# Performance work log

Measured on AMD Instinct MI355X. Metric: run time of the kernel, lower is better.

## Reference

```python
import jax, jax.numpy as jnp
import numpy as np

LENS = 0.4
DECAY = 0.2
THRESH = 0.2
LOG_SIG_MIN, LOG_SIG_MAX = -20.0, 2.0

# Surrogate-gradient spike: forward is heaviside, backward is rectangular window |x|<lens
@jax.custom_vjp
def act_fun(x):
    return (x > 0.0).astype(x.dtype)

def _act_fwd(x):
    return act_fun(x), x

def _act_bwd(x, g):
    return (g * (jnp.abs(x) < LENS).astype(g.dtype),)

act_fun.defvjp(_act_fwd, _act_bwd)


def _xavier(k, shape):
    fan_out, fan_in = shape
    lim = float(np.sqrt(6.0 / (fan_in + fan_out)))
    return jax.random.uniform(k, shape, jnp.float32, -lim, lim)


def setup_inputs() -> dict:
    key = jax.random.key(0)
    ks = jax.random.split(key, 9)
    B, IN, H, A = 4096, 512, 2048, 32
    return {
        "state": jax.random.normal(ks[0], (B, 5, IN), jnp.float32),
        "W_lif": _xavier(ks[1], (H, IN)), "b_lif": jnp.zeros((H,), jnp.float32),
        "W11": _xavier(ks[2], (H, H)), "b11": jnp.zeros((H,), jnp.float32),
        "W12": _xavier(ks[3], (H, H)), "b12": jnp.zeros((H,), jnp.float32),
        "W21": _xavier(ks[4], (H, H)), "b21": jnp.zeros((H,), jnp.float32),
        "W22": _xavier(ks[5], (H, H)), "b22": jnp.zeros((H,), jnp.float32),
        "Wm": _xavier(ks[6], (A, H)), "bm": jnp.zeros((A,), jnp.float32),
        "Wls": _xavier(ks[7], (A, H)), "bls": jnp.zeros((A,), jnp.float32),
    }


def reference(state, W_lif, b_lif, W11, b11, W12, b12, W21, b21, W22, b22, Wm, bm, Wls, bls):
    x_seq = jnp.repeat(state, 3, axis=1)
    # precompute fc(x) for all steps in one GEMM: [B,15,H]
    fc = jnp.einsum('bti,hi->bth', x_seq, W_lif) + b_lif
    B, T, H = fc.shape

    def step(carry, fc_t):
        mem, spike = carry
        mem1 = mem * DECAY * (1.0 - spike) + fc_t
        spike1 = act_fun(mem1 - THRESH)
        return (mem1, spike1), spike1

    init = (jnp.zeros((B, H), fc.dtype), jnp.zeros((B, H), fc.dtype))
    _, spikes = jax.lax.scan(step, init, jnp.swapaxes(fc, 0, 1))  # [T,B,H]
    x = jnp.mean(spikes, axis=0)  # [B,H]

    x1 = jax.nn.relu(x @ W11.T + b11)
    x1 = jax.nn.relu(x1 @ W12.T + b12)
    mean = x1 @ Wm.T + bm

    x2 = jax.nn.relu(x @ W21.T + b21)
    x2 = jax.nn.relu(x2 @ W22.T + b22)
    log_std = jnp.clip(x2 @ Wls.T + bls, LOG_SIG_MIN, LOG_SIG_MAX)
    return mean, log_std
```

## Files before the change

kernel.cpp:

```cpp
#include <hip/hip_runtime.h>
#include <hip/hip_bf16.h>


typedef _Float16 f16;
using f32x4 = __attribute__((ext_vector_type(4))) float;
using f16x8 = __attribute__((ext_vector_type(8))) f16;

#define MFMA16(a, b, c) __builtin_amdgcn_mfma_f32_16x16x32_f16((a), (b), (c), 0, 0, 0)
#define VMW8()  asm volatile("s_waitcnt vmcnt(8)" ::: "memory")
#define VMW4()  asm volatile("s_waitcnt vmcnt(4)" ::: "memory")
#define VMW0()  asm volatile("s_waitcnt vmcnt(0)" ::: "memory")
#define LGKM0() asm volatile("s_waitcnt lgkmcnt(0)" ::: "memory")
#define BARRIER() __builtin_amdgcn_s_barrier()
#define SCHED0() __builtin_amdgcn_sched_barrier(0)

__device__ __forceinline__ void gload16(const void* g, void* l) {
  __builtin_amdgcn_global_load_lds(
      (const __attribute__((address_space(1))) unsigned int*)g,
      (__attribute__((address_space(3))) unsigned int*)l, 16, 0, 0);
}

__global__ __launch_bounds__(256) void cvt_kernel(
    const float* __restrict__ src, f16* __restrict__ dst, int n8)
{
  int i = blockIdx.x * 256 + threadIdx.x;
  if (i >= n8) return;
  const float4* s4 = (const float4*)src;
  float4 a = s4[(size_t)i * 2], b = s4[(size_t)i * 2 + 1];
  f16x8 d;
  d[0] = (f16)a.x; d[1] = (f16)a.y; d[2] = (f16)a.z; d[3] = (f16)a.w;
  d[4] = (f16)b.x; d[5] = (f16)b.y; d[6] = (f16)b.z; d[7] = (f16)b.w;
  *(f16x8*)(dst + (size_t)i * 8) = d;
}

__global__ __launch_bounds__(256) void cvt2_kernel(
    const float* __restrict__ s0, const float* __restrict__ s1,
    f16* __restrict__ d0, f16* __restrict__ d1, int n8each)
{
  int i = blockIdx.x * 256 + threadIdx.x;
  const float* src = (i < n8each) ? s0 : s1;
  f16* dst = (i < n8each) ? d0 : d1;
  int k = (i < n8each) ? i : i - n8each;
  if (k >= n8each) return;
  const float4* s4 = (const float4*)src;
  float4 a = s4[(size_t)k * 2], b = s4[(size_t)k * 2 + 1];
  f16x8 d;
  d[0] = (f16)a.x; d[1] = (f16)a.y; d[2] = (f16)a.z; d[3] = (f16)a.w;
  d[4] = (f16)b.x; d[5] = (f16)b.y; d[6] = (f16)b.z; d[7] = (f16)b.w;
  *(f16x8*)(dst + (size_t)k * 8) = d;
}

__global__ __launch_bounds__(512, 1) void lif256_kernel(
    const f16* __restrict__ S,
    const f16* __restrict__ W,
    const float* __restrict__ bl,
    f16* __restrict__ X)
{
  __shared__ alignas(16) f16 lds[4][128 * 64];

  const int tid = threadIdx.x, wid = tid >> 6, lane = tid & 63;
  const int wg = ((int)blockIdx.x % 8) * 64 + (int)blockIdx.x / 8;
  const int bn = wg & 15, bm = wg >> 4;
  const int b0 = bm * 128, h0 = bn * 128;
  const int wr0 = (wid >> 2) * 64, wc0 = (wid & 3) * 32;
  const int fr = lane & 15, fq = lane >> 4;
  const int sr = tid >> 3, scb = (tid & 7) * 16;

  f32x4 acc[4][2] = {};
  float mem[4][2][4] = {};
  float cnt[4][2][4] = {};

  auto STAGE = [&](int slot, int g) {
    const int s = g >> 3, k0 = (g & 7) * 64;
#pragma unroll
    for (int l = 0; l < 2; ++l) {
      const int row = l * 64 + sr;
      const int c2 = scb ^ ((row & 7) << 4);
      gload16(S + ((size_t)(b0 + row) * 5 + s) * 512 + k0 + (c2 >> 1),
              &lds[slot][l * 4096 + tid * 8]);
    }
#pragma unroll
    for (int l = 0; l < 2; ++l) {
      const int row = l * 64 + sr;
      const int c2 = scb ^ ((row & 7) << 4);
      gload16(W + (size_t)(h0 + row) * 512 + k0 + (c2 >> 1),
              &lds[2 + slot][l * 4096 + tid * 8]);
    }
  };

  auto LDA_ = [&](int slot, int mf, int ks) -> f16x8 {
    const int row = wr0 + mf * 16 + fr;
    const int c = (ks * 64 + fq * 16) ^ ((row & 7) << 4);
    return *(const f16x8*)&lds[slot][row * 64 + (c >> 1)];
  };
  auto LDB_ = [&](int slot, int nf, int ks) -> f16x8 {
    const int row = wc0 + nf * 16 + fr;
    const int c = (ks * 64 + fq * 16) ^ ((row & 7) << 4);
    return *(const f16x8*)&lds[2 + slot][row * 64 + (c >> 1)];
  };

  const float bias[2] = { bl[h0 + wc0 + fr], bl[h0 + wc0 + 16 + fr] };

  STAGE(0, 0);
  STAGE(1, 1);
  VMW4();
  BARRIER();
  SCHED0();

#pragma unroll 2
  for (int g = 0; g < 40; ++g) {
    const int slot = g & 1;

    f16x8 b[2][2], a[2][2];
#pragma unroll
    for (int nf = 0; nf < 2; ++nf) {
      b[nf][0] = LDB_(slot, nf, 0);
      b[nf][1] = LDB_(slot, nf, 1);
    }
#pragma unroll
    for (int i = 0; i < 2; ++i) {
      a[i][0] = LDA_(slot, i, 0);
      a[i][1] = LDA_(slot, i, 1);
    }
    BARRIER(); LGKM0(); SCHED0();
    __builtin_amdgcn_s_setprio(1);
#pragma unroll
    for (int i = 0; i < 2; ++i)
#pragma unroll
      for (int nf = 0; nf < 2; ++nf) {
        acc[i][nf] = MFMA16(a[i][0], b[nf][0], acc[i][nf]);
        acc[i][nf] = MFMA16(a[i][1], b[nf][1], acc[i][nf]);
      }
    __builtin_amdgcn_s_setprio(0);
    BARRIER();

#pragma unroll
    for (int i = 0; i < 2; ++i) {
      a[i][0] = LDA_(slot, 2 + i, 0);
      a[i][1] = LDA_(slot, 2 + i, 1);
    }
    LGKM0(); SCHED0();
    BARRIER();
    if (g + 2 < 40) STAGE(slot, g + 2);
    SCHED0();
    __builtin_amdgcn_s_setprio(1);
#pragma unroll
    for (int i = 0; i < 2; ++i)
#pragma unroll
      for (int nf = 0; nf < 2; ++nf) {
        acc[2 + i][nf] = MFMA16(a[i][0], b[nf][0], acc[2 + i][nf]);
        acc[2 + i][nf] = MFMA16(a[i][1], b[nf][1], acc[2 + i][nf]);
      }
    __builtin_amdgcn_s_setprio(0);

    if ((g & 7) == 7) {
#pragma unroll
      for (int mf = 0; mf < 4; ++mf)
#pragma unroll
        for (int nf = 0; nf < 2; ++nf) {
#pragma unroll
          for (int r = 0; r < 4; ++r) {
            const float fc = acc[mf][nf][r] + bias[nf];
            float m = mem[mf][nf][r], c = cnt[mf][nf][r];
#pragma unroll
            for (int j = 0; j < 3; ++j) {
              m = ((m > 0.2f) ? 0.f : m * 0.2f) + fc;
              c += (m > 0.2f) ? 1.f : 0.f;
            }
            mem[mf][nf][r] = m; cnt[mf][nf][r] = c;
          }
          acc[mf][nf] = f32x4{0.f, 0.f, 0.f, 0.f};
        }
    }

    if (g + 2 < 40)      { VMW4(); }
    else if (g + 1 < 40) { VMW0(); }
    BARRIER();
    SCHED0();
  }

#pragma unroll
  for (int nf = 0; nf < 2; ++nf) {
    const int col = h0 + wc0 + nf * 16 + fr;
#pragma unroll
    for (int mf = 0; mf < 4; ++mf) {
      const int row0 = b0 + wr0 + mf * 16 + fq * 4;
#pragma unroll
      for (int r = 0; r < 4; ++r)
        X[(size_t)(row0 + r) * 2048 + col] = (f16)(cnt[mf][nf][r] / 15.0f);
    }
  }
}

__global__ __launch_bounds__(512, 2) void trunk256_kernel(
    const f16* __restrict__ A0, const f16* __restrict__ A1, int lda,
    const f16* __restrict__ W0, const f16* __restrict__ W1,
    const float* __restrict__ bb0, const float* __restrict__ bb1,
    f16* __restrict__ C0, f16* __restrict__ C1, int ldc,
    int nbm, int nbn_half, int K)
{
  __shared__ alignas(16) f16 lds[4][256 * 64];

  const int tid = threadIdx.x, wid = tid >> 6, lane = tid & 63;
  const int nwg = nbm * nbn_half * 2, q8 = nwg / 8;
  const int wg = ((int)blockIdx.x % 8) * q8 + (int)blockIdx.x / 8;
  const int bmi = wg % nbm, t = wg / nbm;
  const int half = (t >= nbn_half);
  const f16* Ap = half ? A1 : A0;
  const f16* Wp = half ? W1 : W0;
  const float* bias = half ? bb1 : bb0;
  f16* C = half ? C1 : C0;
  const int bm0 = bmi * 256;
  const int bn0 = (half ? t - nbn_half : t) * 256;

  const int wr0 = (wid >> 2) * 128, wc0 = (wid & 3) * 64;
  const int fr = lane & 15, fq = lane >> 4;
  const int sr = tid >> 3, scb = (tid & 7) * 16;

  f32x4 acc[8][4] = {};
  const int NT = K / 64;

  auto STAGE = [&](int slot, int kt) {
    const int k0 = kt * 64;
#pragma unroll
    for (int l = 0; l < 4; ++l) {
      const int row = l * 64 + sr;
      const int c2 = scb ^ ((row & 7) << 4);
      gload16(Ap + (size_t)(bm0 + row) * lda + k0 + (c2 >> 1),
              &lds[slot][l * 4096 + tid * 8]);
    }
#pragma unroll
    for (int l = 0; l < 4; ++l) {
      const int row = l * 64 + sr;
      const int c2 = scb ^ ((row & 7) << 4);
      gload16(Wp + (size_t)(bn0 + row) * K + k0 + (c2 >> 1),
              &lds[2 + slot][l * 4096 + tid * 8]);
    }
  };

  auto LDA_ = [&](int slot, int mf, int ks) -> f16x8 {
    const int row = wr0 + mf * 16 + fr;
    const int c = (ks * 64 + fq * 16) ^ ((row & 7) << 4);
    return *(const f16x8*)&lds[slot][row * 64 + (c >> 1)];
  };
  auto LDB_ = [&](int slot, int nf, int ks) -> f16x8 {
    const int row = wc0 + nf * 16 + fr;
    const int c = (ks * 64 + fq * 16) ^ ((row & 7) << 4);
    return *(const f16x8*)&lds[2 + slot][row * 64 + (c >> 1)];
  };

  STAGE(0, 0);
  STAGE(1, 1);
  VMW8();
  BARRIER();
  SCHED0();

  for (int kt = 0; kt < NT; ++kt) {
    const int slot = kt & 1;
    f16x8 b[4][2], a[2][2];

    auto QUAD = [&](int mbase) {
      __builtin_amdgcn_s_setprio(1);
#pragma unroll
      for (int nf = 0; nf < 4; ++nf) {
        acc[mbase][nf]     = MFMA16(a[0][0], b[nf][0], acc[mbase][nf]);
        acc[mbase][nf]     = MFMA16(a[0][1], b[nf][1], acc[mbase][nf]);
        acc[mbase + 1][nf] = MFMA16(a[1][0], b[nf][0], acc[mbase + 1][nf]);
        acc[mbase + 1][nf] = MFMA16(a[1][1], b[nf][1], acc[mbase + 1][nf]);
      }
      __builtin_amdgcn_s_setprio(0);
    };

#pragma unroll
    for (int nf = 0; nf < 4; ++nf) {
      b[nf][0] = LDB_(slot, nf, 0);
      b[nf][1] = LDB_(slot, nf, 1);
    }
#pragma unroll
    for (int i = 0; i < 2; ++i) { a[i][0] = LDA_(slot, i, 0); a[i][1] = LDA_(slot, i, 1); }
    BARRIER(); LGKM0(); SCHED0();
    QUAD(0);
    BARRIER();

#pragma unroll
    for (int i = 0; i < 2; ++i) { a[i][0] = LDA_(slot, 2 + i, 0); a[i][1] = LDA_(slot, 2 + i, 1); }
    BARRIER(); LGKM0(); SCHED0();
    QUAD(2);
    BARRIER();

#pragma unroll
    for (int i = 0; i < 2; ++i) { a[i][0] = LDA_(slot, 4 + i, 0); a[i][1] = LDA_(slot, 4 + i, 1); }
    BARRIER(); LGKM0(); SCHED0();
    QUAD(4);
    BARRIER();

#pragma unroll
    for (int i = 0; i < 2; ++i) { a[i][0] = LDA_(slot, 6 + i, 0); a[i][1] = LDA_(slot, 6 + i, 1); }
    LGKM0(); SCHED0();
    BARRIER();
    if (kt + 2 < NT) STAGE(slot, kt + 2);
    SCHED0();
    QUAD(6);
    if (kt + 2 < NT)      { VMW8(); }
    else if (kt + 1 < NT) { VMW0(); }
    BARRIER();
    SCHED0();
  }

#pragma unroll
  for (int nf = 0; nf < 4; ++nf) {
    const int col = bn0 + wc0 + nf * 16 + fr;
    const float bv = bias[col];
#pragma unroll
    for (int m = 0; m < 8; ++m) {
      const int row0 = bm0 + wr0 + m * 16 + fq * 4;
#pragma unroll
      for (int r = 0; r < 4; ++r) {
        float v = fmaxf(acc[m][nf][r] + bv, 0.f);
        C[(size_t)(row0 + r) * ldc + col] = (f16)v;
      }
    }
  }
}

__global__ __launch_bounds__(256) void head_kernel(
    const f16* __restrict__ H1, const f16* __restrict__ H2,
    const f16* __restrict__ Wm, const float* __restrict__ bm,
    const f16* __restrict__ Wls, const float* __restrict__ bls,
    float* __restrict__ OUT, int M, int K)
{
  const int tid = threadIdx.x, wid = tid >> 6, lane = tid & 63;
  const int m0 = blockIdx.x * 64 + wid * 16;
  const int kb = (lane >> 4) * 8, fr = lane & 15, fq = lane >> 4;

  f32x4 a1[2] = {}, a2[2] = {};
  for (int k0 = 0; k0 < K; k0 += 32) {
    f16x8 f1 = *(const f16x8*)&H1[(size_t)(m0 + fr) * K + k0 + kb];
    f16x8 f2 = *(const f16x8*)&H2[(size_t)(m0 + fr) * K + k0 + kb];
#pragma unroll
    for (int n = 0; n < 2; ++n) {
      f16x8 wm = *(const f16x8*)&Wm[(size_t)(n * 16 + fr) * K + k0 + kb];
      f16x8 wl = *(const f16x8*)&Wls[(size_t)(n * 16 + fr) * K + k0 + kb];
      a1[n] = MFMA16(f1, wm, a1[n]);
      a2[n] = MFMA16(f2, wl, a2[n]);
    }
  }

#pragma unroll
  for (int n = 0; n < 2; ++n) {
    const int col = n * 16 + fr;
    const float bvm = bm[col];
    const float bvl = bls[col];
#pragma unroll
    for (int r = 0; r < 4; ++r) {
      const int row = m0 + fq * 4 + r;
      OUT[(size_t)row * 32 + col] = a1[n][r] + bvm;
      float lv = a2[n][r] + bvl;
      OUT[(size_t)M * 32 + (size_t)row * 32 + col] = fminf(fmaxf(lv, -20.f), 2.f);
    }
  }
}

extern "C" void kernel_launch(void* const* d_in, const int* in_sizes, int n_in,
                              void* d_out, int out_size, void* d_ws, size_t ws_size,
                              hipStream_t stream) {
  const float* state = (const float*)d_in[0];
  const float* W_lif = (const float*)d_in[1];
  const float* b_lif = (const float*)d_in[2];
  const float* W11   = (const float*)d_in[3];
  const float* b11   = (const float*)d_in[4];
  const float* W12   = (const float*)d_in[5];
  const float* b12   = (const float*)d_in[6];
  const float* W21   = (const float*)d_in[7];
  const float* b21   = (const float*)d_in[8];
  const float* W22   = (const float*)d_in[9];
  const float* b22   = (const float*)d_in[10];
  const float* Wm    = (const float*)d_in[11];
  const float* bm    = (const float*)d_in[12];
  const float* Wls   = (const float*)d_in[13];
  const float* bls   = (const float*)d_in[14];
  float* out = (float*)d_out;

  const int B = 4096, IN = 512, H = 2048;
  char* ws = (char*)d_ws;
  f16* x    = (f16*)(ws);
  f16* h1   = (f16*)(ws + 16777216);
  f16* h2   = (f16*)(ws + 33554432);
  f16* s16  = (f16*)(ws + 50331648);
  f16* wl16 = (f16*)(ws + 71303168);
  f16* w11h = (f16*)(ws + 50331648);
  f16* w21h = (f16*)(ws + 58720256);
  f16* h22  = (f16*)(ws + 50331648);
  f16* w12h = (f16*)(ws + 67108864);
  f16* w22h = (f16*)(ws + 75497472);
  f16* wmh  = (f16*)(ws + 67108864);
  f16* wlsh = (f16*)(ws + 67239936);
  f16* h12  = x;

  cvt_kernel<<<(B * 5 * IN / 8) / 256, 256, 0, stream>>>(state, s16, B * 5 * IN / 8);
  cvt_kernel<<<(H * IN / 8) / 256, 256, 0, stream>>>(W_lif, wl16, H * IN / 8);

  lif256_kernel<<<512, 512, 0, stream>>>(s16, wl16, b_lif, x);

  cvt2_kernel<<<2 * (H * H / 8) / 256, 256, 0, stream>>>(W11, W21, w11h, w21h, H * H / 8);
  trunk256_kernel<<<256, 512, 0, stream>>>(x, x, H, w11h, w21h, b11, b21,
                                           h1, h2, H, 16, 8, H);

  cvt2_kernel<<<2 * (H * H / 8) / 256, 256, 0, stream>>>(W12, W22, w12h, w22h, H * H / 8);
  trunk256_kernel<<<256, 512, 0, stream>>>(h1, h2, H, w12h, w22h, b12, b22,
                                           h12, h22, H, 16, 8, H);

  cvt2_kernel<<<2 * (32 * H / 8) / 256, 256, 0, stream>>>(Wm, Wls, wmh, wlsh, 32 * H / 8);
  head_kernel<<<B / 64, 256, 0, stream>>>(h12, h22, wmh, bm, wlsh, bls, out, B, H);
}
```

Baseline: 290.6 us.

## Merge conversion kernels, precompute LDS/global addresses, restructure trunk GEMM loop

Several separate changes land together. The fp32-to-fp16 conversions are merged into fewer launches: state and W_lif share one kernel, and all four trunk weights share another. Both GEMM kernels now precompute LDS and global base pointers outside the loop instead of recomputing swizzled addresses each iteration. The trunk GEMM inner loop drops most intra-iteration barriers, double-buffers the A fragments so LDS reads overlap MFMAs, and unrolls by two. The fewer barriers and extra registers in flight could change occupancy or scheduling behavior.

```diff
diff --git a/kernel.cpp b/kernel.cpp
--- a/kernel.cpp
+++ b/kernel.cpp
@@ -20,17 +20,37 @@
       (__attribute__((address_space(3))) unsigned int*)l, 16, 0, 0);
 }
 
-__global__ __launch_bounds__(256) void cvt_kernel(
-    const float* __restrict__ src, f16* __restrict__ dst, int n8)
-{
-  int i = blockIdx.x * 256 + threadIdx.x;
-  if (i >= n8) return;
-  const float4* s4 = (const float4*)src;
-  float4 a = s4[(size_t)i * 2], b = s4[(size_t)i * 2 + 1];
+__device__ __forceinline__ void cvt8(const float4& a, const float4& b, f16* dst) {
   f16x8 d;
   d[0] = (f16)a.x; d[1] = (f16)a.y; d[2] = (f16)a.z; d[3] = (f16)a.w;
   d[4] = (f16)b.x; d[5] = (f16)b.y; d[6] = (f16)b.z; d[7] = (f16)b.w;
-  *(f16x8*)(dst + (size_t)i * 8) = d;
+  *(f16x8*)dst = d;
+}
+
+__global__ __launch_bounds__(256) void cvt2b_kernel(
+    const float* __restrict__ s0, f16* __restrict__ d0, int n8a,
+    const float* __restrict__ s1, f16* __restrict__ d1, int n8b)
+{
+  int i = blockIdx.x * 256 + threadIdx.x;
+  const float* src; f16* dst; int k;
+  if (i < n8a) { src = s0; dst = d0; k = i; }
+  else { k = i - n8a; if (k >= n8b) return; src = s1; dst = d1; }
+  const float4* s4 = (const float4*)src;
+  float4 a = s4[(size_t)k * 2], b = s4[(size_t)k * 2 + 1];
+  cvt8(a, b, dst + (size_t)k * 8);
+}
+
+__global__ __launch_bounds__(256) void cvt4_kernel(
+    const float* __restrict__ w0, const float* __restrict__ w1,
+    const float* __restrict__ w2, const float* __restrict__ w3,
+    f16* __restrict__ dst)
+{
+  int i = blockIdx.x * 256 + threadIdx.x;
+  int which = i >> 19, k = i & 524287;
+  const float* src = (which == 0) ? w0 : (which == 1) ? w1 : (which == 2) ? w2 : w3;
+  const float4* s4 = (const float4*)src;
+  float4 a = s4[(size_t)k * 2], b = s4[(size_t)k * 2 + 1];
+  cvt8(a, b, dst + (size_t)i * 8);
 }
 
 __global__ __launch_bounds__(256) void cvt2_kernel(
@@ -44,10 +64,7 @@
   if (k >= n8each) return;
   const float4* s4 = (const float4*)src;
   float4 a = s4[(size_t)k * 2], b = s4[(size_t)k * 2 + 1];
-  f16x8 d;
-  d[0] = (f16)a.x; d[1] = (f16)a.y; d[2] = (f16)a.z; d[3] = (f16)a.w;
-  d[4] = (f16)b.x; d[5] = (f16)b.y; d[6] = (f16)b.z; d[7] = (f16)b.w;
-  *(f16x8*)(dst + (size_t)k * 8) = d;
+  cvt8(a, b, dst + (size_t)k * 8);
 }
 
 __global__ __launch_bounds__(512, 1) void lif256_kernel(
@@ -70,33 +87,33 @@
   float mem[4][2][4] = {};
   float cnt[4][2][4] = {};
 
+  char* Lb = (char*)&lds[0][0];
+  const int xsw = (fr & 7) << 4;
+  const int x0 = (fq * 16) ^ xsw;
+  const int x1 = (64 + fq * 16) ^ xsw;
+  char* const pA0 = Lb + (wr0 + fr) * 128 + x0;
+  char* const pA1 = Lb + (wr0 + fr) * 128 + x1;
+  char* const pB0 = Lb + 32768 + (wc0 + fr) * 128 + x0;
+  char* const pB1 = Lb + 32768 + (wc0 + fr) * 128 + x1;
+
+  const f16* sBase[2]; const f16* wBase[2];
+#pragma unroll
+  for (int l = 0; l < 2; ++l) {
+    const int row = l * 64 + sr;
+    const int c2 = scb ^ ((row & 7) << 4);
+    sBase[l] = S + (size_t)(b0 + row) * 2560 + (c2 >> 1);
+    wBase[l] = W + (size_t)(h0 + row) * 512 + (c2 >> 1);
+  }
+
   auto STAGE = [&](int slot, int g) {
-    const int s = g >> 3, k0 = (g & 7) * 64;
-#pragma unroll
-    for (int l = 0; l < 2; ++l) {
-      const int row = l * 64 + sr;
-      const int c2 = scb ^ ((row & 7) << 4);
-      gload16(S + ((size_t)(b0 + row) * 5 + s) * 512 + k0 + (c2 >> 1),
-              &lds[slot][l * 4096 + tid * 8]);
-    }
-#pragma unroll
-    for (int l = 0; l < 2; ++l) {
-      const int row = l * 64 + sr;
-      const int c2 = scb ^ ((row & 7) << 4);
-      gload16(W + (size_t)(h0 + row) * 512 + k0 + (c2 >> 1),
-              &lds[2 + slot][l * 4096 + tid * 8]);
-    }
-  };
-
-  auto LDA_ = [&](int slot, int mf, int ks) -> f16x8 {
-    const int row = wr0 + mf * 16 + fr;
-    const int c = (ks * 64 + fq * 16) ^ ((row & 7) << 4);
-    return *(const f16x8*)&lds[slot][row * 64 + (c >> 1)];
-  };
-  auto LDB_ = [&](int slot, int nf, int ks) -> f16x8 {
-    const int row = wc0 + nf * 16 + fr;
-    const int c = (ks * 64 + fq * 16) ^ ((row & 7) << 4);
-    return *(const f16x8*)&lds[2 + slot][row * 64 + (c >> 1)];
+    const int koff = (g >> 3) * 512 + (g & 7) * 64;
+    const int kw = (g & 7) * 64;
+#pragma unroll
+    for (int l = 0; l < 2; ++l)
+      gload16(sBase[l] + koff, Lb + slot * 16384 + l * 8192 + tid * 16);
+#pragma unroll
+    for (int l = 0; l < 2; ++l)
+      gload16(wBase[l] + kw, Lb + 32768 + slot * 16384 + l * 8192 + tid * 16);
   };
 
   const float bias[2] = { bl[h0 + wc0 + fr], bl[h0 + wc0 + 16 + fr] };
@@ -110,17 +127,18 @@
 #pragma unroll 2
   for (int g = 0; g < 40; ++g) {
     const int slot = g & 1;
+    const int so = slot * 16384;
 
     f16x8 b[2][2], a[2][2];
 #pragma unroll
     for (int nf = 0; nf < 2; ++nf) {
-      b[nf][0] = LDB_(slot, nf, 0);
-      b[nf][1] = LDB_(slot, nf, 1);
-    }
-#pragma unroll
-    for (int i = 0; i < 2; ++i) {
-      a[i][0] = LDA_(slot, i, 0);
-      a[i][1] = LDA_(slot, i, 1);
+      b[nf][0] = *(const f16x8*)(pB0 + so + nf * 2048);
+      b[nf][1] = *(const f16x8*)(pB1 + so + nf * 2048);
+    }
+#pragma unroll
+    for (int i = 0; i < 2; ++i) {
+      a[i][0] = *(const f16x8*)(pA0 + so + i * 2048);
+      a[i][1] = *(const f16x8*)(pA1 + so + i * 2048);
     }
     BARRIER(); LGKM0(); SCHED0();
     __builtin_amdgcn_s_setprio(1);
@@ -136,8 +154,8 @@
 
 #pragma unroll
     for (int i = 0; i < 2; ++i) {
-      a[i][0] = LDA_(slot, 2 + i, 0);
-      a[i][1] = LDA_(slot, 2 + i, 1);
+      a[i][0] = *(const f16x8*)(pA0 + so + (2 + i) * 2048);
+      a[i][1] = *(const f16x8*)(pA1 + so + (2 + i) * 2048);
     }
     LGKM0(); SCHED0();
     BARRIER();
@@ -220,33 +238,32 @@
   f32x4 acc[8][4] = {};
   const int NT = K / 64;
 
+  char* Lb = (char*)&lds[0][0];
+  const int xsw = (fr & 7) << 4;
+  const int x0 = (fq * 16) ^ xsw;
+  const int x1 = (64 + fq * 16) ^ xsw;
+  char* const pA0 = Lb + (wr0 + fr) * 128 + x0;
+  char* const pA1 = Lb + (wr0 + fr) * 128 + x1;
+  char* const pB0 = Lb + 65536 + (wc0 + fr) * 128 + x0;
+  char* const pB1 = Lb + 65536 + (wc0 + fr) * 128 + x1;
+
+  const f16* aBase[4]; const f16* wBase[4];
+#pragma unroll
+  for (int l = 0; l < 4; ++l) {
+    const int row = l * 64 + sr;
+    const int c2 = scb ^ ((row & 7) << 4);
+    aBase[l] = Ap + (size_t)(bm0 + row) * lda + (c2 >> 1);
+    wBase[l] = Wp + (size_t)(bn0 + row) * K + (c2 >> 1);
+  }
+
   auto STAGE = [&](int slot, int kt) {
-    const int k0 = kt * 64;
-#pragma unroll
-    for (int l = 0; l < 4; ++l) {
-      const int row = l * 64 + sr;
-      const int c2 = scb ^ ((row & 7) << 4);
-      gload16(Ap + (size_t)(bm0 + row) * lda + k0 + (c2 >> 1),
-              &lds[slot][l * 4096 + tid * 8]);
-    }
-#pragma unroll
-    for (int l = 0; l < 4; ++l) {
-      const int row = l * 64 + sr;
-      const int c2 = scb ^ ((row & 7) << 4);
-      gload16(Wp + (size_t)(bn0 + row) * K + k0 + (c2 >> 1),
-              &lds[2 + slot][l * 4096 + tid * 8]);
-    }
-  };
-
-  auto LDA_ = [&](int slot, int mf, int ks) -> f16x8 {
-    const int row = wr0 + mf * 16 + fr;
-    const int c = (ks * 64 + fq * 16) ^ ((row & 7) << 4);
-    return *(const f16x8*)&lds[slot][row * 64 + (c >> 1)];
-  };
-  auto LDB_ = [&](int slot, int nf, int ks) -> f16x8 {
-    const int row = wc0 + nf * 16 + fr;
-    const int c = (ks * 64 + fq * 16) ^ ((row & 7) << 4);
-    return *(const f16x8*)&lds[2 + slot][row * 64 + (c >> 1)];
+    const int koff = kt * 64;
+#pragma unroll
+    for (int l = 0; l < 4; ++l)
+      gload16(aBase[l] + koff, Lb + slot * 32768 + l * 8192 + tid * 16);
+#pragma unroll
+    for (int l = 0; l < 4; ++l)
+      gload16(wBase[l] + koff, Lb + 65536 + slot * 32768 + l * 8192 + tid * 16);
   };
 
   STAGE(0, 0);
@@ -255,11 +272,25 @@
   BARRIER();
   SCHED0();
 
+#pragma unroll 2
   for (int kt = 0; kt < NT; ++kt) {
     const int slot = kt & 1;
-    f16x8 b[4][2], a[2][2];
-
-    auto QUAD = [&](int mbase) {
+    const int so = slot * 32768;
+
+    f16x8 b[4][2];
+#pragma unroll
+    for (int nf = 0; nf < 4; ++nf) {
+      b[nf][0] = *(const f16x8*)(pB0 + so + nf * 2048);
+      b[nf][1] = *(const f16x8*)(pB1 + so + nf * 2048);
+    }
+    f16x8 a0[2][2], a1[2][2];
+#pragma unroll
+    for (int i = 0; i < 2; ++i) {
+      a0[i][0] = *(const f16x8*)(pA0 + so + i * 2048);
+      a0[i][1] = *(const f16x8*)(pA1 + so + i * 2048);
+    }
+
+    auto QUAD = [&](int mbase, f16x8 (&a)[2][2]) {
       __builtin_amdgcn_s_setprio(1);
 #pragma unroll
       for (int nf = 0; nf < 4; ++nf) {
@@ -272,37 +303,35 @@
     };
 
 #pragma unroll
-    for (int nf = 0; nf < 4; ++nf) {
-      b[nf][0] = LDB_(slot, nf, 0);
-      b[nf][1] = LDB_(slot, nf, 1);
-    }
-#pragma unroll
-    for (int i = 0; i < 2; ++i) { a[i][0] = LDA_(slot, i, 0); a[i][1] = LDA_(slot, i, 1); }
-    BARRIER(); LGKM0(); SCHED0();
-    QUAD(0);
+    for (int i = 0; i < 2; ++i) {
+      a1[i][0] = *(const f16x8*)(pA0 + so + (2 + i) * 2048);
+      a1[i][1] = *(const f16x8*)(pA1 + so + (2 + i) * 2048);
+    }
+    QUAD(0, a0);
+#pragma unroll
+    for (int i = 0; i < 2; ++i) {
+      a0[i][0] = *(const f16x8*)(pA0 + so + (4 + i) * 2048);
+      a0[i][1] = *(const f16x8*)(pA1 + so + (4 + i) * 2048);
+    }
+    QUAD(2, a1);
+#pragma unroll
+    for (int i = 0; i < 2; ++i) {
+      a1[i][0] = *(const f16x8*)(pA0 + so + (6 + i) * 2048);
+      a1[i][1] = *(const f16x8*)(pA1 + so + (6 + i) * 2048);
+    }
+    QUAD(4, a0);
+    QUAD(6, a1);
+
+    LGKM0();
     BARRIER();
-
-#pragma unroll
-    for (int i = 0; i < 2; ++i) { a[i][0] = LDA_(slot, 2 + i, 0); a[i][1] = LDA_(slot, 2 + i, 1); }
-    BARRIER(); LGKM0(); SCHED0();
-    QUAD(2);
-    BARRIER();
-
-#pragma unroll
-    for (int i = 0; i < 2; ++i) { a[i][0] = LDA_(slot, 4 + i, 0); a[i][1] = LDA_(slot, 4 + i, 1); }
-    BARRIER(); LGKM0(); SCHED0();
-    QUAD(4);
-    BARRIER();
-
-#pragma unroll
-    for (int i = 0; i < 2; ++i) { a[i][0] = LDA_(slot, 6 + i, 0); a[i][1] = LDA_(slot, 6 + i, 1); }
-    LGKM0(); SCHED0();
-    BARRIER();
-    if (kt + 2 < NT) STAGE(slot, kt + 2);
     SCHED0();
-    QUAD(6);
-    if (kt + 2 < NT)      { VMW8(); }
-    else if (kt + 1 < NT) { VMW0(); }
+    if (kt + 2 < NT) {
+      STAGE(slot, kt + 2);
+      SCHED0();
+      VMW8();
+    } else if (kt + 1 < NT) {
+      VMW0();
+    }
     BARRIER();
     SCHED0();
   }
@@ -388,25 +417,26 @@
   f16* h2   = (f16*)(ws + 33554432);
   f16* s16  = (f16*)(ws + 50331648);
   f16* wl16 = (f16*)(ws + 71303168);
+  f16* w4   = (f16*)(ws + 50331648);
   f16* w11h = (f16*)(ws + 50331648);
   f16* w21h = (f16*)(ws + 58720256);
-  f16* h22  = (f16*)(ws + 50331648);
   f16* w12h = (f16*)(ws + 67108864);
   f16* w22h = (f16*)(ws + 75497472);
+  f16* h22  = (f16*)(ws + 50331648);
   f16* wmh  = (f16*)(ws + 67108864);
   f16* wlsh = (f16*)(ws + 67239936);
   f16* h12  = x;
 
-  cvt_kernel<<<(B * 5 * IN / 8) / 256, 256, 0, stream>>>(state, s16, B * 5 * IN / 8);
-  cvt_kernel<<<(H * IN / 8) / 256, 256, 0, stream>>>(W_lif, wl16, H * IN / 8);
+  const int n8s = B * 5 * IN / 8, n8w = H * IN / 8;
+  cvt2b_kernel<<<(n8s + n8w + 255) / 256, 256, 0, stream>>>(
+      state, s16, n8s, W_lif, wl16, n8w);
 
   lif256_kernel<<<512, 512, 0, stream>>>(s16, wl16, b_lif, x);
 
-  cvt2_kernel<<<2 * (H * H / 8) / 256, 256, 0, stream>>>(W11, W21, w11h, w21h, H * H / 8);
+  cvt4_kernel<<<4 * 524288 / 256, 256, 0, stream>>>(W11, W21, W12, W22, w4);
+
   trunk256_kernel<<<256, 512, 0, stream>>>(x, x, H, w11h, w21h, b11, b21,
                                            h1, h2, H, 16, 8, H);
-
-  cvt2_kernel<<<2 * (H * H / 8) / 256, 256, 0, stream>>>(W12, W22, w12h, w22h, H * H / 8);
   trunk256_kernel<<<256, 512, 0, stream>>>(h1, h2, H, w12h, w22h, b12, b22,
                                            h12, h22, H, 16, 8, H);
 
```

After: 278.0 us. 4.3% less time.
